# Kernel tuning notes

Measured on AMD Instinct MI355X. Metric: run time of the kernel, lower is better.

Reference implementation:

```python
import jax, jax.numpy as jnp
import numpy as np

B, N, F, H = 8, 2048, 64, 1

def setup_inputs() -> dict:
    key = jax.random.key(0)
    k1, k2, k3, k4 = jax.random.split(key, 4)
    return {
        "encode": jax.random.normal(k1, (B, N, F), dtype=jnp.float32),
        "kernel": jax.random.normal(k2, (F, H, F), dtype=jnp.float32) * 0.1,
        "attn_kernel_self": jax.random.normal(k3, (F, H, 1), dtype=jnp.float32) * 0.1,
        "attn_kernel_neighs": jax.random.normal(k4, (F, H, 1), dtype=jnp.float32) * 0.1,
    }

def reference(encode, kernel, attn_kernel_self, attn_kernel_neighs):
    # project: [B,N,F] x [F,H,F] -> [B,N,H,F]
    h = jnp.einsum('bni,iho->bnho', encode, kernel)
    # per-node scalar scores: [B,N,H,1]
    a_self = jnp.einsum('bnhi,iho->bnho', h, attn_kernel_self)
    a_neigh = jnp.einsum('bnhi,iho->bnho', h, attn_kernel_neighs)
    # transpose last three axes (...ABC -> ...CBA): [B,1,H,N]
    a_neigh_t = jnp.transpose(a_neigh, (0, 3, 2, 1))
    # broadcast-sum -> [B,N,H,N] dense logits, leaky_relu(alpha=0.2), softmax over neighbors
    logits = jax.nn.leaky_relu(a_self + a_neigh_t, negative_slope=0.2)
    coef = jax.nn.softmax(logits, axis=-1)
    # mean over heads (axis=2) -> [B,N,N]
    return jnp.mean(coef, axis=2)
```

## Files before the change

### kernel.cpp

```cpp
#include <hip/hip_runtime.h>

#define BB 8
#define NN 2048
#define FF 64

__global__ void fold_kernel(const float* __restrict__ kmat,
                            const float* __restrict__ aks,
                            const float* __restrict__ akn,
                            float* __restrict__ ws, float* __restrict__ wn) {
    int i = threadIdx.x;
    float s = 0.f, t = 0.f;
    #pragma unroll
    for (int o = 0; o < FF; ++o) {
        float k = kmat[i * FF + o];
        s += k * aks[o];
        t += k * akn[o];
    }
    ws[i] = s;
    wn[i] = t;
}

__global__ __launch_bounds__(256) void scores_kernel(const float* __restrict__ enc,
                                                     const float* __restrict__ ws,
                                                     const float* __restrict__ wn,
                                                     float* __restrict__ S,
                                                     float* __restrict__ T) {
    int g = blockIdx.x * blockDim.x + threadIdx.x;
    if (g >= BB * NN) return;
    const float4* e4 = (const float4*)(enc + (size_t)g * FF);
    const float4* w4 = (const float4*)ws;
    const float4* v4 = (const float4*)wn;
    float s = 0.f, t = 0.f;
    #pragma unroll
    for (int j = 0; j < FF / 4; ++j) {
        float4 e = e4[j];
        float4 w = w4[j];
        float4 v = v4[j];
        s += e.x * w.x + e.y * w.y + e.z * w.z + e.w * w.w;
        t += e.x * v.x + e.y * v.y + e.z * v.z + e.w * v.w;
    }
    S[g] = s;
    T[g] = t;
}

__device__ __forceinline__ float waveMax(float v) {
    #pragma unroll
    for (int o = 32; o > 0; o >>= 1) v = fmaxf(v, __shfl_xor(v, o, 64));
    return v;
}
__device__ __forceinline__ float waveSum(float v) {
    #pragma unroll
    for (int o = 32; o > 0; o >>= 1) v += __shfl_xor(v, o, 64);
    return v;
}

__global__ __launch_bounds__(256) void softmax_kernel(const float* __restrict__ S,
                                                      const float* __restrict__ T,
                                                      float* __restrict__ out) {
    const int row = blockIdx.x;
    const int b   = row >> 11;
    const int tid = threadIdx.x;

    const float s = S[row];
    const float4* t4 = (const float4*)(T + (size_t)b * NN);

    float4 ta = t4[tid];
    float4 tb = t4[tid + 256];

    auto lk = [](float x) { return x > 0.f ? x : 0.2f * x; };
    float l[8];
    l[0] = lk(s + ta.x); l[1] = lk(s + ta.y); l[2] = lk(s + ta.z); l[3] = lk(s + ta.w);
    l[4] = lk(s + tb.x); l[5] = lk(s + tb.y); l[6] = lk(s + tb.z); l[7] = lk(s + tb.w);

    float m8 = l[0];
    #pragma unroll
    for (int k = 1; k < 8; ++k) m8 = fmaxf(m8, l[k]);
    m8 = waveMax(m8);
    __shared__ float redm[4];
    __shared__ float reds[4];
    const int wave = tid >> 6, lane = tid & 63;
    if (lane == 0) redm[wave] = m8;
    __syncthreads();
    const float rowmax = fmaxf(fmaxf(redm[0], redm[1]), fmaxf(redm[2], redm[3]));

    float e[8];
    float ls = 0.f;
    #pragma unroll
    for (int k = 0; k < 8; ++k) {
        e[k] = __expf(l[k] - rowmax);
        ls += e[k];
    }
    ls = waveSum(ls);
    if (lane == 0) reds[wave] = ls;
    __syncthreads();
    const float inv = 1.f / (reds[0] + reds[1] + reds[2] + reds[3]);

    float4* o4 = (float4*)(out + (size_t)row * NN);
    float4 oa, ob;
    oa.x = e[0] * inv; oa.y = e[1] * inv; oa.z = e[2] * inv; oa.w = e[3] * inv;
    ob.x = e[4] * inv; ob.y = e[5] * inv; ob.z = e[6] * inv; ob.w = e[7] * inv;
    o4[tid]       = oa;
    o4[tid + 256] = ob;
}

extern "C" void kernel_launch(void* const* d_in, const int* in_sizes, int n_in,
                              void* d_out, int out_size, void* d_ws, size_t ws_size,
                              hipStream_t stream) {
    const float* enc  = (const float*)d_in[0];
    const float* kmat = (const float*)d_in[1];
    const float* aks  = (const float*)d_in[2];
    const float* akn  = (const float*)d_in[3];
    float* out = (float*)d_out;

    float* W  = (float*)d_ws;
    float* ws = W;
    float* wn = W + 64;
    float* S  = W + 128;
    float* T  = W + 128 + BB * NN;

    fold_kernel<<<1, 64, 0, stream>>>(kmat, aks, akn, ws, wn);
    scores_kernel<<<(BB * NN + 255) / 256, 256, 0, stream>>>(enc, ws, wn, S, T);
    softmax_kernel<<<BB * NN, 256, 0, stream>>>(S, T, out);
}
```

Baseline: 35.55 us.

## Fuse weight fold into scores kernel and use one wave per softmax row

The separate fold kernel is merged into the scores kernel: every block recomputes the folded attention weights into shared memory, which removes one kernel launch at the cost of redundant tiny work per block. The softmax kernel now handles one row per wave (four rows per block), so the reductions are wave shuffles only and the shared-memory barriers are gone. Output rows are written with nontemporal stores to limit cache pollution from the large output. Each lane now keeps 32 values in registers, which raises register pressure.

```diff
diff --git a/kernel.cpp b/kernel.cpp
--- a/kernel.cpp
+++ b/kernel.cpp
@@ -4,38 +4,39 @@
 #define NN 2048
 #define FF 64
 
-__global__ void fold_kernel(const float* __restrict__ kmat,
-                            const float* __restrict__ aks,
-                            const float* __restrict__ akn,
-                            float* __restrict__ ws, float* __restrict__ wn) {
-    int i = threadIdx.x;
-    float s = 0.f, t = 0.f;
-    #pragma unroll
-    for (int o = 0; o < FF; ++o) {
-        float k = kmat[i * FF + o];
-        s += k * aks[o];
-        t += k * akn[o];
+typedef float f32x4 __attribute__((ext_vector_type(4)));
+
+__global__ __launch_bounds__(256) void scores_fused(const float* __restrict__ enc,
+                                                    const float* __restrict__ kmat,
+                                                    const float* __restrict__ aks,
+                                                    const float* __restrict__ akn,
+                                                    float* __restrict__ S,
+                                                    float* __restrict__ T) {
+    __shared__ float ws[FF], wn[FF];
+    const int tid = threadIdx.x;
+    if (tid < FF) {
+        float s = 0.f, t = 0.f;
+        #pragma unroll
+        for (int o = 0; o < FF; ++o) {
+            float k = kmat[tid * FF + o];
+            s += k * aks[o];
+            t += k * akn[o];
+        }
+        ws[tid] = s;
+        wn[tid] = t;
     }
-    ws[i] = s;
-    wn[i] = t;
-}
+    __syncthreads();
 
-__global__ __launch_bounds__(256) void scores_kernel(const float* __restrict__ enc,
-                                                     const float* __restrict__ ws,
-                                                     const float* __restrict__ wn,
-                                                     float* __restrict__ S,
-                                                     float* __restrict__ T) {
-    int g = blockIdx.x * blockDim.x + threadIdx.x;
-    if (g >= BB * NN) return;
-    const float4* e4 = (const float4*)(enc + (size_t)g * FF);
-    const float4* w4 = (const float4*)ws;
-    const float4* v4 = (const float4*)wn;
+    const int g = blockIdx.x * 256 + tid;
+    const f32x4* e4 = (const f32x4*)(enc + (size_t)g * FF);
+    const f32x4* w4 = (const f32x4*)ws;
+    const f32x4* v4 = (const f32x4*)wn;
     float s = 0.f, t = 0.f;
     #pragma unroll
     for (int j = 0; j < FF / 4; ++j) {
-        float4 e = e4[j];
-        float4 w = w4[j];
-        float4 v = v4[j];
+        f32x4 e = e4[j];
+        f32x4 w = w4[j];
+        f32x4 v = v4[j];
         s += e.x * w.x + e.y * w.y + e.z * w.z + e.w * w.w;
         t += e.x * v.x + e.y * v.y + e.z * v.z + e.w * v.w;
     }
@@ -57,50 +58,45 @@
 __global__ __launch_bounds__(256) void softmax_kernel(const float* __restrict__ S,
                                                       const float* __restrict__ T,
                                                       float* __restrict__ out) {
-    const int row = blockIdx.x;
-    const int b   = row >> 11;
-    const int tid = threadIdx.x;
+    const int wave = threadIdx.x >> 6;
+    const int lane = threadIdx.x & 63;
+    const int row  = blockIdx.x * 4 + wave;
+    const int b    = row >> 11;
 
     const float s = S[row];
-    const float4* t4 = (const float4*)(T + (size_t)b * NN);
-
-    float4 ta = t4[tid];
-    float4 tb = t4[tid + 256];
+    const f32x4* t4 = (const f32x4*)(T + (size_t)b * NN);
 
     auto lk = [](float x) { return x > 0.f ? x : 0.2f * x; };
-    float l[8];
-    l[0] = lk(s + ta.x); l[1] = lk(s + ta.y); l[2] = lk(s + ta.z); l[3] = lk(s + ta.w);
-    l[4] = lk(s + tb.x); l[5] = lk(s + tb.y); l[6] = lk(s + tb.z); l[7] = lk(s + tb.w);
 
-    float m8 = l[0];
+    f32x4 l[8];
+    float m = -3.4e38f;
     #pragma unroll
-    for (int k = 1; k < 8; ++k) m8 = fmaxf(m8, l[k]);
-    m8 = waveMax(m8);
-    __shared__ float redm[4];
-    __shared__ float reds[4];
-    const int wave = tid >> 6, lane = tid & 63;
-    if (lane == 0) redm[wave] = m8;
-    __syncthreads();
-    const float rowmax = fmaxf(fmaxf(redm[0], redm[1]), fmaxf(redm[2], redm[3]));
+    for (int j = 0; j < 8; ++j) {
+        f32x4 t = t4[lane + 64 * j];
+        l[j].x = lk(s + t.x); l[j].y = lk(s + t.y);
+        l[j].z = lk(s + t.z); l[j].w = lk(s + t.w);
+        m = fmaxf(m, fmaxf(fmaxf(l[j].x, l[j].y), fmaxf(l[j].z, l[j].w)));
+    }
+    m = waveMax(m);
 
-    float e[8];
     float ls = 0.f;
     #pragma unroll
-    for (int k = 0; k < 8; ++k) {
-        e[k] = __expf(l[k] - rowmax);
-        ls += e[k];
+    for (int j = 0; j < 8; ++j) {
+        l[j].x = __expf(l[j].x - m); l[j].y = __expf(l[j].y - m);
+        l[j].z = __expf(l[j].z - m); l[j].w = __expf(l[j].w - m);
+        ls += (l[j].x + l[j].y) + (l[j].z + l[j].w);
     }
     ls = waveSum(ls);
-    if (lane == 0) reds[wave] = ls;
-    __syncthreads();
-    const float inv = 1.f / (reds[0] + reds[1] + reds[2] + reds[3]);
+    const float inv = 1.f / ls;
 
-    float4* o4 = (float4*)(out + (size_t)row * NN);
-    float4 oa, ob;
-    oa.x = e[0] * inv; oa.y = e[1] * inv; oa.z = e[2] * inv; oa.w = e[3] * inv;
-    ob.x = e[4] * inv; ob.y = e[5] * inv; ob.z = e[6] * inv; ob.w = e[7] * inv;
-    o4[tid]       = oa;
-    o4[tid + 256] = ob;
+    f32x4* o4 = (f32x4*)(out + (size_t)row * NN);
+    #pragma unroll
+    for (int j = 0; j < 8; ++j) {
+        f32x4 o;
+        o.x = l[j].x * inv; o.y = l[j].y * inv;
+        o.z = l[j].z * inv; o.w = l[j].w * inv;
+        __builtin_nontemporal_store(o, &o4[lane + 64 * j]);
+    }
 }
 
 extern "C" void kernel_launch(void* const* d_in, const int* in_sizes, int n_in,
@@ -112,13 +108,10 @@
     const float* akn  = (const float*)d_in[3];
     float* out = (float*)d_out;
 
-    float* W  = (float*)d_ws;
-    float* ws = W;
-    float* wn = W + 64;
-    float* S  = W + 128;
-    float* T  = W + 128 + BB * NN;
+    float* W = (float*)d_ws;
+    float* S = W;
+    float* T = W + BB * NN;
 
-    fold_kernel<<<1, 64, 0, stream>>>(kmat, aks, akn, ws, wn);
-    scores_kernel<<<(BB * NN + 255) / 256, 256, 0, stream>>>(enc, ws, wn, S, T);
-    softmax_kernel<<<BB * NN, 256, 0, stream>>>(S, T, out);
+    scores_fused<<<BB * NN / 256, 256, 0, stream>>>(enc, kmat, aks, akn, S, T);
+    softmax_kernel<<<BB * NN / 4, 256, 0, stream>>>(S, T, out);
 }
```

Result: faster. 33.32 us (-6.3%).
